# Performance work log

Hardware: AMD Instinct MI355X
Metric: run time of the kernel (lower is better)

## Reference

```python
import jax, jax.numpy as jnp
import numpy as np

N_QUBITS = 12
N_LAYERS = 6
BATCH = 512

def _apply_1q(state, U, wire):
    # state: (B, 2, ..., 2); U: (2,2) shared across batch or (B,2,2) batched
    ax = wire + 1
    s = jnp.moveaxis(state, ax, -1)
    if U.ndim == 3:
        s = jnp.einsum('bij,b...j->b...i', U, s)
    else:
        s = jnp.einsum('ij,b...j->b...i', U, s)
    return jnp.moveaxis(s, -1, ax)

def _apply_cnot(state, ctrl, tgt):
    ca, ta = ctrl + 1, tgt + 1
    s0 = jnp.take(state, 0, axis=ca)
    s1 = jnp.take(state, 1, axis=ca)
    ta2 = ta - 1 if ta > ca else ta  # axis shift after removing ctrl axis
    s1 = jnp.flip(s1, axis=ta2)      # X on target where control == 1
    return jnp.stack([s0, s1], axis=ca)

def _rot_matrix(phi, theta, omega):
    # PennyLane Rot = RZ(omega) @ RY(theta) @ RZ(phi)
    c = jnp.cos(theta / 2)
    s = jnp.sin(theta / 2)
    a = jnp.exp(-0.5j * (phi + omega)) * c
    b = -jnp.exp(0.5j * (phi - omega)) * s
    cc = jnp.exp(-0.5j * (phi - omega)) * s
    d = jnp.exp(0.5j * (phi + omega)) * c
    return jnp.stack([jnp.stack([a, b]), jnp.stack([cc, d])]).astype(jnp.complex64)

def _layer(state, w):
    # w: (N_QUBITS, 3) -> per-wire Rot, then CNOT ring
    for j in range(N_QUBITS):
        state = _apply_1q(state, _rot_matrix(w[j, 0], w[j, 1], w[j, 2]), j)
    for j in range(N_QUBITS):
        state = _apply_cnot(state, j, (j + 1) % N_QUBITS)
    return state

def _circuit(feats, weights):
    B = feats.shape[0]
    state = jnp.zeros((B,) + (2,) * N_QUBITS, jnp.complex64)
    state = state.at[(slice(None),) + (0,) * N_QUBITS].set(1.0)  # |0...0>
    # AngleEmbedding rotation='X': batched RX(feats[:, j]) on wire j
    for j in range(N_QUBITS):
        half = feats[:, j] / 2
        c = jnp.cos(half).astype(jnp.complex64)
        m = (-1j) * jnp.sin(half).astype(jnp.complex64)
        U = jnp.stack([jnp.stack([c, m], -1), jnp.stack([m, c], -1)], -2)  # (B,2,2)
        state = _apply_1q(state, U, j)
    lay = jax.checkpoint(_layer)
    for i in range(N_LAYERS):
        state = lay(state, weights[i])
    # <Z_0>: marginal probability on wire 0
    probs = jnp.sum(jnp.abs(state) ** 2, axis=tuple(range(2, N_QUBITS + 1)))  # (B, 2)
    return probs[:, 0] - probs[:, 1]

def setup_inputs():
    key = jax.random.key(0)
    k1, k2 = jax.random.split(key)
    x = jax.random.normal(k1, (BATCH, 3, 224, 224), jnp.float32)
    weights = jax.random.uniform(k2, (N_LAYERS, N_QUBITS, 3), jnp.float32, 0.0, 2.0 * np.pi)
    bias = jnp.zeros((), jnp.float32)
    return {"x": x, "weights": weights, "bias": bias}

def reference(x, weights, bias):
    B = x.shape[0]
    feats = x.reshape(B, -1)[:, :N_QUBITS]
    q_out = _circuit(feats, weights)
    return (q_out + bias)[:, None]  # (B, 1)
```

## Files before the change

kernel.cpp:

```cpp
#include <hip/hip_runtime.h>

#define NLAYERS 6
#define XROW 150528

typedef float v2f __attribute__((ext_vector_type(2)));


__global__ void qnn_prep(const float* __restrict__ w, float* __restrict__ coef) {
    const int g = threadIdx.x;
    if (g < NLAYERS * 12) {
        const float phi = w[g*3+0], th = w[g*3+1], om = w[g*3+2];
        const float ct = cosf(0.5f*th), st = sinf(0.5f*th);
        const float sp = 0.5f*(phi+om), dm = 0.5f*(phi-om);
        const float csp = cosf(sp), ssp = sinf(sp);
        const float cdm = cosf(dm), sdm = sinf(dm);
        float* c = coef + g*8;
        c[0] =  csp*ct; c[1] = -ssp*ct;
        c[2] = -cdm*st; c[3] = -sdm*st;
        c[4] =  cdm*st; c[5] = -sdm*st;
        c[6] =  csp*ct; c[7] =  ssp*ct;
    }
}

__device__ __forceinline__ v2f cfma(float s, v2f a, v2f c) {
    v2f sv = {s, s};
    return __builtin_elementwise_fma(sv, a, c);
}

template<int BP>
__device__ __forceinline__ void rot_local(v2f (&v)[16], const float* __restrict__ cf) {
    const float ar = cf[0], ai = cf[1], br = cf[2], bi = cf[3];
    const float cr = cf[4], ci = cf[5], dr = cf[6], di = cf[7];
    #pragma unroll
    for (int l0 = 0; l0 < 16; ++l0) {
        if (!(l0 & (1 << BP))) {
            const int l1 = l0 | (1 << BP);
            const v2f u0 = v[l0], u1 = v[l1];
            const v2f t0 = {-u0.y, u0.x};
            const v2f t1 = {-u1.y, u1.x};
            const v2f sar = {ar, ar}, scr = {cr, cr};
            v[l0] = cfma(bi, t1, cfma(br, u1, cfma(ai, t0, sar * u0)));
            v[l1] = cfma(di, t1, cfma(dr, u1, cfma(ci, t0, scr * u0)));
        }
    }
}

#define SWAP_AMP(A,B) { v2f t_ = v[A]; v[A] = v[B]; v[B] = t_; }
#define RING_CNOTS_LOCAL() \
    SWAP_AMP(8,12) SWAP_AMP(9,13) SWAP_AMP(10,14) SWAP_AMP(11,15) \
    SWAP_AMP(4,6)  SWAP_AMP(5,7)  SWAP_AMP(12,14) SWAP_AMP(13,15) \
    SWAP_AMP(2,3)  SWAP_AMP(6,7)  SWAP_AMP(10,11) SWAP_AMP(14,15)

__global__ __launch_bounds__(256, 2) void qnn_kernel(
    const float* __restrict__ x,
    const float* __restrict__ coef,
    const float* __restrict__ bias,
    float* __restrict__ out)
{
    __shared__ v2f st[2][4096];
    __shared__ float partial[4];

    const int tid  = threadIdx.x;
    const int lane = tid & 63;
    const int wv   = tid >> 6;
    const int b    = blockIdx.x;

    v2f v[16];
    int pb = 0;

    const float* xb = x + (size_t)b * XROW;
    float fc[12], fs[12];
    #pragma unroll
    for (int j = 0; j < 12; ++j) {
        const float h = xb[j] * 0.5f;
        fc[j] = __cosf(h);
        fs[j] = __sinf(h);
    }
    float pr = 1.f, pi_ = 0.f;
    #pragma unroll
    for (int j = 4; j < 12; ++j) {
        const int bit = (j < 10) ? ((lane >> (9 - j)) & 1)
                                 : ((j == 10) ? ((wv >> 1) & 1) : (wv & 1));
        const float nr = bit ? (pi_ * fs[j]) : (pr * fc[j]);
        const float ni = bit ? (-pr * fs[j]) : (pi_ * fc[j]);
        pr = nr; pi_ = ni;
    }
    v[0] = (v2f){pr, pi_};
    #pragma unroll
    for (int bb = 0; bb < 4; ++bb) {
        const int wire = 3 - bb;
        const float cc = fc[wire], ss = fs[wire];
        const int m = 1 << bb;
        #pragma unroll
        for (int l = 0; l < 8; ++l) {
            if (l < m) {
                const float r = v[l].x, q = v[l].y;
                v[l + m] = (v2f){q * ss, -r * ss};
                v[l]     = (v2f){r * cc,  q * cc};
            }
        }
    }

    for (int layer = 0; layer < NLAYERS; ++layer) {
        const float* cl = coef + layer * 96;

        if (layer) {
            v2f* S = st[pb];
            #pragma unroll
            for (int l = 0; l < 16; ++l)
                S[(l << 8) | (tid ^ l ^ wv)] = v[l];
            __syncthreads();
            {
                const int l_old = ((lane & 3) << 2) | wv;
                const int w_old = (lane >> 2) & 3;
                const int n_lo  = (lane >> 4) & 3;
                const int fold  = (wv & 1) << 3;
                #pragma unroll
                for (int l = 0; l < 16; ++l) {
                    const int lp2   = l ^ fold;
                    const int n_old = (lp2 << 2) | n_lo;
                    const int t_old = (w_old << 6) | n_old;
                    v[l] = S[(l_old << 8) | (t_old ^ l_old ^ w_old)];
                }
            }
            pb ^= 1;
        }

        rot_local<3>(v, cl + 0*8);
        rot_local<2>(v, cl + 1*8);
        rot_local<1>(v, cl + 2*8);
        rot_local<0>(v, cl + 3*8);
        RING_CNOTS_LOCAL();

        {
            v2f* S = st[pb];
            #pragma unroll
            for (int l = 0; l < 16; ++l)
                S[(l << 8) | (tid ^ (l << 2))] = v[l];
            __syncthreads();
            const int l_old = (lane >> 2) & 0xF;
            const int n_lo  = lane & 3;
            #pragma unroll
            for (int l = 0; l < 16; ++l) {
                const int n_old = (l << 2) | n_lo;
                const int t_old = (wv << 6) | n_old;
                v[l] = S[(l_old << 8) | (t_old ^ (l_old << 2))];
            }
            pb ^= 1;
        }

        rot_local<3>(v, cl + 4*8);
        rot_local<2>(v, cl + 5*8);
        rot_local<1>(v, cl + 6*8);
        rot_local<0>(v, cl + 7*8);
        {
            const bool sel = (lane >> 2) & 1;
            #pragma unroll
            for (int l = 0; l < 8; ++l) {
                const v2f a0 = v[l], a1 = v[l + 8];
                v[l]     = sel ? a1 : a0;
                v[l + 8] = sel ? a0 : a1;
            }
        }
        RING_CNOTS_LOCAL();

        {
            v2f* S = st[pb];
            #pragma unroll
            for (int l = 0; l < 16; ++l) {
                const int sw = ((l & 1) << 3) | ((l & 2) << 1) | ((l & 4) >> 1) | ((l & 8) >> 3);
                S[(l << 8) | (tid ^ sw)] = v[l];
            }
            __syncthreads();
            const int l_old = ((lane & 3) << 2) | wv;
            const int swo = ((l_old & 1) << 3) | ((l_old & 2) << 1)
                          | ((l_old & 4) >> 1) | ((l_old & 8) >> 3);
            const int n_hi = ((lane >> 2) & 0xF) << 2;
            #pragma unroll
            for (int l = 0; l < 16; ++l) {
                const int n_old = n_hi | (l >> 2);
                const int w_old = l & 3;
                const int t_old = (w_old << 6) | n_old;
                v[l] = S[(l_old << 8) | (t_old ^ swo)];
            }
            pb ^= 1;
        }

        rot_local<3>(v, cl + 8*8);
        rot_local<2>(v, cl + 9*8);
        rot_local<1>(v, cl + 10*8);
        rot_local<0>(v, cl + 11*8);
        {
            const bool sel = wv & 1;
            #pragma unroll
            for (int l = 0; l < 8; ++l) {
                const v2f a0 = v[l], a1 = v[l + 8];
                v[l]     = sel ? a1 : a0;
                v[l + 8] = sel ? a0 : a1;
            }
        }
        RING_CNOTS_LOCAL();
    }

    float acc = 0.f;
    #pragma unroll
    for (int l = 0; l < 16; ++l) {
        const float p = v[l].x * v[l].x + v[l].y * v[l].y;
        acc += ((((lane >> 5) ^ l) & 1) ? -p : p);
    }
    #pragma unroll
    for (int off = 32; off > 0; off >>= 1)
        acc += __shfl_down(acc, off, 64);
    if (lane == 0) partial[wv] = acc;
    __syncthreads();
    if (tid == 0)
        out[b] = partial[0] + partial[1] + partial[2] + partial[3] + bias[0];
}

extern "C" void kernel_launch(void* const* d_in, const int* in_sizes, int n_in,
                              void* d_out, int out_size, void* d_ws, size_t ws_size,
                              hipStream_t stream) {
    const float* x    = (const float*)d_in[0];
    const float* wts  = (const float*)d_in[1];
    const float* bias = (const float*)d_in[2];
    float* out  = (float*)d_out;
    float* coef = (float*)d_ws;
    qnn_prep<<<1, 128, 0, stream>>>(wts, coef);
    qnn_kernel<<<out_size, 256, 0, stream>>>(x, coef, bias, out);
}
```

Baseline: 371.3 us.

## Split state across 512 threads with 8 amplitudes each and 3-wire passes

Redistributes the 4096-amplitude state vector from 256 threads holding 16 amplitudes each to 512 threads holding 8 each. Each layer becomes four passes of three local-wire rotations, with a shared-memory transpose between passes, instead of three passes of four wires. This halves register use per thread and doubles the threads per batch element to raise parallelism and occupancy. The cost is more LDS exchanges and barriers per layer: four passes instead of three, plus one more at layer boundaries.

```diff
diff --git a/kernel.cpp b/kernel.cpp
--- a/kernel.cpp
+++ b/kernel.cpp
@@ -28,11 +28,11 @@
 }
 
 template<int BP>
-__device__ __forceinline__ void rot_local(v2f (&v)[16], const float* __restrict__ cf) {
+__device__ __forceinline__ void rot_local(v2f (&v)[8], const float* __restrict__ cf) {
     const float ar = cf[0], ai = cf[1], br = cf[2], bi = cf[3];
     const float cr = cf[4], ci = cf[5], dr = cf[6], di = cf[7];
     #pragma unroll
-    for (int l0 = 0; l0 < 16; ++l0) {
+    for (int l0 = 0; l0 < 8; ++l0) {
         if (!(l0 & (1 << BP))) {
             const int l1 = l0 | (1 << BP);
             const v2f u0 = v[l0], u1 = v[l1];
@@ -47,26 +47,29 @@
 
 #define SWAP_AMP(A,B) { v2f t_ = v[A]; v[A] = v[B]; v[B] = t_; }
 #define RING_CNOTS_LOCAL() \
-    SWAP_AMP(8,12) SWAP_AMP(9,13) SWAP_AMP(10,14) SWAP_AMP(11,15) \
-    SWAP_AMP(4,6)  SWAP_AMP(5,7)  SWAP_AMP(12,14) SWAP_AMP(13,15) \
-    SWAP_AMP(2,3)  SWAP_AMP(6,7)  SWAP_AMP(10,11) SWAP_AMP(14,15)
+    SWAP_AMP(4,6) SWAP_AMP(5,7) SWAP_AMP(2,3) SWAP_AMP(6,7)
 
-__global__ __launch_bounds__(256, 2) void qnn_kernel(
+__global__ __launch_bounds__(512, 4) void qnn_kernel(
     const float* __restrict__ x,
     const float* __restrict__ coef,
     const float* __restrict__ bias,
     float* __restrict__ out)
 {
     __shared__ v2f st[2][4096];
-    __shared__ float partial[4];
+    __shared__ float partial[8];
 
     const int tid  = threadIdx.x;
     const int lane = tid & 63;
     const int wv   = tid >> 6;
     const int b    = blockIdx.x;
 
-    v2f v[16];
+    v2f v[8];
     int pb = 0;
+
+    const int wbase = (lane << 3) | (wv ^ ((lane >> 1) & 7));
+    const int rbase = wv << 9;
+    const int u     = lane >> 3;
+    const int w7    = lane & 7;
 
     const float* xb = x + (size_t)b * XROW;
     float fc[12], fs[12];
@@ -78,21 +81,21 @@
     }
     float pr = 1.f, pi_ = 0.f;
     #pragma unroll
-    for (int j = 4; j < 12; ++j) {
-        const int bit = (j < 10) ? ((lane >> (9 - j)) & 1)
-                                 : ((j == 10) ? ((wv >> 1) & 1) : (wv & 1));
+    for (int j = 3; j < 12; ++j) {
+        const int bit = (j < 9) ? ((lane >> (8 - j)) & 1)
+                                : ((wv >> (11 - j)) & 1);
         const float nr = bit ? (pi_ * fs[j]) : (pr * fc[j]);
         const float ni = bit ? (-pr * fs[j]) : (pi_ * fc[j]);
         pr = nr; pi_ = ni;
     }
     v[0] = (v2f){pr, pi_};
     #pragma unroll
-    for (int bb = 0; bb < 4; ++bb) {
-        const int wire = 3 - bb;
+    for (int bb = 0; bb < 3; ++bb) {
+        const int wire = 2 - bb;
         const float cc = fc[wire], ss = fs[wire];
         const int m = 1 << bb;
         #pragma unroll
-        for (int l = 0; l < 8; ++l) {
+        for (int l = 0; l < 4; ++l) {
             if (l < m) {
                 const float r = v[l].x, q = v[l].y;
                 v[l + m] = (v2f){q * ss, -r * ss};
@@ -104,107 +107,43 @@
     for (int layer = 0; layer < NLAYERS; ++layer) {
         const float* cl = coef + layer * 96;
 
-        if (layer) {
-            v2f* S = st[pb];
-            #pragma unroll
-            for (int l = 0; l < 16; ++l)
-                S[(l << 8) | (tid ^ l ^ wv)] = v[l];
-            __syncthreads();
-            {
-                const int l_old = ((lane & 3) << 2) | wv;
-                const int w_old = (lane >> 2) & 3;
-                const int n_lo  = (lane >> 4) & 3;
-                const int fold  = (wv & 1) << 3;
+        #pragma unroll
+        for (int p = 0; p < 4; ++p) {
+            if (layer || p) {
+                const int fold = (p == 0) ? ((wv & 1) << 2) : 0;
+                v2f* S = st[pb];
                 #pragma unroll
-                for (int l = 0; l < 16; ++l) {
-                    const int lp2   = l ^ fold;
-                    const int n_old = (lp2 << 2) | n_lo;
-                    const int t_old = (w_old << 6) | n_old;
-                    v[l] = S[(l_old << 8) | (t_old ^ l_old ^ w_old)];
+                for (int l = 0; l < 8; ++l)
+                    S[(l << 9) | wbase] = v[l];
+                __syncthreads();
+                #pragma unroll
+                for (int l = 0; l < 8; ++l) {
+                    const int ol = ((l ^ fold) << 3) | u;
+                    v[l] = S[rbase | (ol << 3) | (w7 ^ ((ol >> 1) & 7))];
+                }
+                pb ^= 1;
+            }
+
+            rot_local<2>(v, cl + (3 * p + 0) * 8);
+            rot_local<1>(v, cl + (3 * p + 1) * 8);
+            rot_local<0>(v, cl + (3 * p + 2) * 8);
+
+            if (p) {
+                const bool sel = wv & 1;
+                #pragma unroll
+                for (int l = 0; l < 4; ++l) {
+                    const v2f a0 = v[l], a1 = v[l + 4];
+                    v[l]     = sel ? a1 : a0;
+                    v[l + 4] = sel ? a0 : a1;
                 }
             }
-            pb ^= 1;
+            RING_CNOTS_LOCAL();
         }
-
-        rot_local<3>(v, cl + 0*8);
-        rot_local<2>(v, cl + 1*8);
-        rot_local<1>(v, cl + 2*8);
-        rot_local<0>(v, cl + 3*8);
-        RING_CNOTS_LOCAL();
-
-        {
-            v2f* S = st[pb];
-            #pragma unroll
-            for (int l = 0; l < 16; ++l)
-                S[(l << 8) | (tid ^ (l << 2))] = v[l];
-            __syncthreads();
-            const int l_old = (lane >> 2) & 0xF;
-            const int n_lo  = lane & 3;
-            #pragma unroll
-            for (int l = 0; l < 16; ++l) {
-                const int n_old = (l << 2) | n_lo;
-                const int t_old = (wv << 6) | n_old;
-                v[l] = S[(l_old << 8) | (t_old ^ (l_old << 2))];
-            }
-            pb ^= 1;
-        }
-
-        rot_local<3>(v, cl + 4*8);
-        rot_local<2>(v, cl + 5*8);
-        rot_local<1>(v, cl + 6*8);
-        rot_local<0>(v, cl + 7*8);
-        {
-            const bool sel = (lane >> 2) & 1;
-            #pragma unroll
-            for (int l = 0; l < 8; ++l) {
-                const v2f a0 = v[l], a1 = v[l + 8];
-                v[l]     = sel ? a1 : a0;
-                v[l + 8] = sel ? a0 : a1;
-            }
-        }
-        RING_CNOTS_LOCAL();
-
-        {
-            v2f* S = st[pb];
-            #pragma unroll
-            for (int l = 0; l < 16; ++l) {
-                const int sw = ((l & 1) << 3) | ((l & 2) << 1) | ((l & 4) >> 1) | ((l & 8) >> 3);
-                S[(l << 8) | (tid ^ sw)] = v[l];
-            }
-            __syncthreads();
-            const int l_old = ((lane & 3) << 2) | wv;
-            const int swo = ((l_old & 1) << 3) | ((l_old & 2) << 1)
-                          | ((l_old & 4) >> 1) | ((l_old & 8) >> 3);
-            const int n_hi = ((lane >> 2) & 0xF) << 2;
-            #pragma unroll
-            for (int l = 0; l < 16; ++l) {
-                const int n_old = n_hi | (l >> 2);
-                const int w_old = l & 3;
-                const int t_old = (w_old << 6) | n_old;
-                v[l] = S[(l_old << 8) | (t_old ^ swo)];
-            }
-            pb ^= 1;
-        }
-
-        rot_local<3>(v, cl + 8*8);
-        rot_local<2>(v, cl + 9*8);
-        rot_local<1>(v, cl + 10*8);
-        rot_local<0>(v, cl + 11*8);
-        {
-            const bool sel = wv & 1;
-            #pragma unroll
-            for (int l = 0; l < 8; ++l) {
-                const v2f a0 = v[l], a1 = v[l + 8];
-                v[l]     = sel ? a1 : a0;
-                v[l + 8] = sel ? a0 : a1;
-            }
-        }
-        RING_CNOTS_LOCAL();
     }
 
     float acc = 0.f;
     #pragma unroll
-    for (int l = 0; l < 16; ++l) {
+    for (int l = 0; l < 8; ++l) {
         const float p = v[l].x * v[l].x + v[l].y * v[l].y;
         acc += ((((lane >> 5) ^ l) & 1) ? -p : p);
     }
@@ -213,8 +152,12 @@
         acc += __shfl_down(acc, off, 64);
     if (lane == 0) partial[wv] = acc;
     __syncthreads();
-    if (tid == 0)
-        out[b] = partial[0] + partial[1] + partial[2] + partial[3] + bias[0];
+    if (tid == 0) {
+        float s = 0.f;
+        #pragma unroll
+        for (int i = 0; i < 8; ++i) s += partial[i];
+        out[b] = s + bias[0];
+    }
 }
 
 extern "C" void kernel_launch(void* const* d_in, const int* in_sizes, int n_in,
@@ -226,5 +169,5 @@
     float* out  = (float*)d_out;
     float* coef = (float*)d_ws;
     qnn_prep<<<1, 128, 0, stream>>>(wts, coef);
-    qnn_kernel<<<out_size, 256, 0, stream>>>(x, coef, bias, out);
+    qnn_kernel<<<out_size, 512, 0, stream>>>(x, coef, bias, out);
 }
```

Result: no change. 370.3 us (-0.3%).
